# Performance work log

Measured on AMD Instinct MI355X. Metric: run time of the kernel, lower is better.

Reference implementation:

```python
import jax, jax.numpy as jnp
import numpy as np

H, D, K = 8, 512, 64
EPS = 1e-12


def _l2norm(x):
    # F.normalize(p=2, dim=-1): x / max(||x||_2, eps)
    n = jnp.sqrt(jnp.sum(x * x, axis=-1, keepdims=True))
    return x / jnp.maximum(n, EPS)


def setup_inputs() -> dict:
    key = jax.random.key(0)
    ks = jax.random.split(key, 8)
    S, B = 1024, 16
    scale = 1.0 / np.sqrt(D)
    return {
        "query": jax.random.normal(ks[0], (S, B, D), dtype=jnp.float32),
        "key": jax.random.normal(ks[1], (S, B, D), dtype=jnp.float32),
        "value": jax.random.normal(ks[2], (S, B, D), dtype=jnp.float32),
        # stacked per-head projection weights, torch Linear convention [out,in]
        "WQ": jax.random.uniform(ks[3], (H, K, D), jnp.float32, -scale, scale),
        "WK": jax.random.uniform(ks[4], (H, K, D), jnp.float32, -scale, scale),
        "WV": jax.random.uniform(ks[5], (H, K, D), jnp.float32, -scale, scale),
        "Wout": jax.random.uniform(ks[6], (D, H * K), jnp.float32,
                                   -1.0 / np.sqrt(H * K), 1.0 / np.sqrt(H * K)),
    }


def reference(query, key, value, WQ, WK, WV, Wout):
    temp = K ** 0.5
    # project all heads at once: [S,B,D] x [H,K,D] -> [B,H,S,K]
    wq = _l2norm(jnp.einsum("sbd,hkd->bhsk", query, WQ))
    wk = _l2norm(jnp.einsum("sbd,hkd->bhsk", key, WK))
    wv = _l2norm(jnp.einsum("sbd,hkd->bhsk", value, WV))
    # cosine-similarity attention scores [B,H,Sq,Sk]
    scores = jnp.einsum("bhsk,bhtk->bhst", wq, wk) / temp
    aff = jax.nn.softmax(scores, axis=-1)
    out = jnp.einsum("bhst,bhtk->bhsk", aff, wv)  # [B,H,S,K]
    # concat heads -> [S,B,H*K] (matches torch per-head concat on last dim)
    Sq, B = query.shape[0], query.shape[1]
    concat = out.transpose(2, 0, 1, 3).reshape(Sq, B, H * K)
    return concat @ Wout.T  # [S,B,D]
```

## Files before the change

kernel.cpp:

```cpp
#include <hip/hip_runtime.h>
#include <cstdint>
#include <cstddef>

typedef unsigned int u32;
typedef unsigned short u16;
typedef __attribute__((ext_vector_type(8))) short short8;
typedef __attribute__((ext_vector_type(4))) float f32x4;

#define S_LEN 1024
#define BATCH 16
#define NHEAD 8
#define DMODEL 512
#define KHD 64
#define NROW (S_LEN * BATCH)

__device__ __forceinline__ u16 f2bf(float f) {
    u32 u = __float_as_uint(f);
    return (u16)((u + 0x7fffu + ((u >> 16) & 1u)) >> 16);
}

__device__ __forceinline__ void gl_lds16(const void* g, void* l) {
    __builtin_amdgcn_global_load_lds(
        (const __attribute__((address_space(1))) void*)(uintptr_t)g,
        (__attribute__((address_space(3))) void*)(uintptr_t)l, 16, 0, 0);
}

__global__ __launch_bounds__(256) void wcvt_kernel(
    const float* __restrict__ WQ, const float* __restrict__ WK,
    const float* __restrict__ WV, const float* __restrict__ Wo,
    u16* __restrict__ dst)
{
    const int m = blockIdx.y;
    const float* __restrict__ src = (m == 0) ? WQ : (m == 1) ? WK : (m == 2) ? WV : Wo;
    const int idx = (blockIdx.x * 256 + threadIdx.x) * 4;
    const float4 v = *(const float4*)(src + idx);
    u16 r[4];
    r[0] = f2bf(v.x); r[1] = f2bf(v.y); r[2] = f2bf(v.z); r[3] = f2bf(v.w);
    *(uint2*)(dst + (size_t)m * DMODEL * DMODEL + idx) = *(uint2*)r;
}

template<int M>
__global__ __launch_bounds__(256) void gemm_kernel(
    const float* __restrict__ A0,
    const float* __restrict__ A1,
    const u16* __restrict__ Wb,
    u16* __restrict__ outN)
{
    __shared__ __align__(16) u16 Alds[128 * 64];
    __shared__ __align__(16) u16 Blds[128 * 64];

    const int tid  = threadIdx.x;
    const int wave = tid >> 6;
    const int lane = tid & 63;
    const int m16  = lane & 15;
    const int quad = lane >> 4;
    const int wm   = wave >> 1;
    const int wn   = wave & 1;
    const int n0   = blockIdx.y * 128;
    const int row0 = blockIdx.x * 128;
    const int z    = (M == 1) ? blockIdx.z : 0;
    const int bb   = (M == 2) ? blockIdx.z : 0;

    const float* __restrict__ A32 =
        (M == 1) ? (z ? A1 : A0) : (A0 + (size_t)bb * DMODEL);
    const size_t astr = (M == 2) ? (size_t)BATCH * DMODEL : (size_t)DMODEL;
    const u16* __restrict__ B = Wb + ((M == 1) ? (size_t)z * DMODEL * DMODEL : 0);

    f32x4 acc[4][4] = {};

    const int brow   = lane >> 3;
    const int bchunk = (lane & 7) ^ brow;
    const int acf    = lane & 7;

    for (int kt = 0; kt < DMODEL; kt += 64) {
        __syncthreads();
        {
            const u16* bp = B + (size_t)(n0 + wave * 32 + brow) * DMODEL + kt + bchunk * 8;
            u16* lb = &Blds[(wave * 32) * 64];
            float4 av[8];
#pragma unroll
            for (int j = 0; j < 8; j++) {
                const int rl = wave * 32 + (j & 3) * 8 + brow;
                const int cf = (j >> 2) * 8 + acf;
                av[j] = *(const float4*)(A32 + (size_t)(row0 + rl) * astr + kt + cf * 4);
            }
#pragma unroll
            for (int j = 0; j < 4; j++)
                gl_lds16(bp + (size_t)j * 8 * DMODEL, lb + j * 8 * 64);
#pragma unroll
            for (int j = 0; j < 8; j++) {
                const int rl = wave * 32 + (j & 3) * 8 + brow;
                const int cf = (j >> 2) * 8 + acf;
                u32 lo, hi;
                asm("v_cvt_pk_bf16_f32 %0, %1, %2" : "=v"(lo) : "v"(av[j].x), "v"(av[j].y));
                asm("v_cvt_pk_bf16_f32 %0, %1, %2" : "=v"(hi) : "v"(av[j].z), "v"(av[j].w));
                uint2 pk; pk.x = lo; pk.y = hi;
                *(uint2*)&Alds[rl * 64 + (((cf >> 1) ^ (rl & 7)) << 3) + ((cf & 1) << 2)] = pk;
            }
        }
        __syncthreads();

#pragma unroll
        for (int half = 0; half < 2; half++) {
            short8 af[4], bfr[4];
#pragma unroll
            for (int mt = 0; mt < 4; mt++)
                af[mt] = *(const short8*)&Alds[(wm * 64 + mt * 16 + m16) * 64 +
                                               (((half << 2) + quad) ^ (m16 & 7)) * 8];
#pragma unroll
            for (int nt = 0; nt < 4; nt++)
                bfr[nt] = *(const short8*)&Blds[(wn * 64 + nt * 16 + m16) * 64 +
                                                (((half << 2) + quad) ^ (m16 & 7)) * 8];
#pragma unroll
            for (int mt = 0; mt < 4; mt++)
#pragma unroll
                for (int nt = 0; nt < 4; nt++)
                    acc[mt][nt] = __builtin_amdgcn_mfma_f32_16x16x32_bf16(af[mt], bfr[nt], acc[mt][nt], 0, 0, 0);
        }
    }

    if (M == 1) {
        const int h = (n0 >> 6) + wn;
        u16* outZ = outN + (size_t)z * BATCH * NHEAD * S_LEN * KHD;
#pragma unroll
        for (int mt = 0; mt < 4; mt++) {
#pragma unroll
            for (int r = 0; r < 4; r++) {
                float ss = 0.0f;
#pragma unroll
                for (int nt = 0; nt < 4; nt++) ss += acc[mt][nt][r] * acc[mt][nt][r];
                ss += __shfl_xor(ss, 1);
                ss += __shfl_xor(ss, 2);
                ss += __shfl_xor(ss, 4);
                ss += __shfl_xor(ss, 8);
                const float sc = 1.0f / fmaxf(sqrtf(ss), 1e-12f);
                const int i = row0 + wm * 64 + mt * 16 + quad * 4 + r;
                const int s = i >> 4, b = i & 15;
                u16* op = outN + (size_t)z * BATCH * NHEAD * S_LEN * KHD +
                          (((size_t)b * NHEAD + h) * S_LEN + s) * KHD;
                (void)outZ;
#pragma unroll
                for (int nt = 0; nt < 4; nt++)
                    op[nt * 16 + m16] = f2bf(acc[mt][nt][r] * sc);
            }
        }
    } else {
        const int h = (n0 >> 6) + wn;
#pragma unroll
        for (int mt = 0; mt < 4; mt++) {
            float scl[4];
#pragma unroll
            for (int r = 0; r < 4; r++) {
                float ss = 0.0f;
#pragma unroll
                for (int nt = 0; nt < 4; nt++) ss += acc[mt][nt][r] * acc[mt][nt][r];
                ss += __shfl_xor(ss, 1);
                ss += __shfl_xor(ss, 2);
                ss += __shfl_xor(ss, 4);
                ss += __shfl_xor(ss, 8);
                scl[r] = 1.0f / fmaxf(sqrtf(ss), 1e-12f);
            }
            const int sbase = row0 + wm * 64 + mt * 16 + quad * 4;
#pragma unroll
            for (int nt = 0; nt < 4; nt++) {
                const int vcol = nt * 16 + m16;
                uint2 pk;
                pk.x = (u32)f2bf(acc[mt][nt][0] * scl[0]) |
                       ((u32)f2bf(acc[mt][nt][1] * scl[1]) << 16);
                pk.y = (u32)f2bf(acc[mt][nt][2] * scl[2]) |
                       ((u32)f2bf(acc[mt][nt][3] * scl[3]) << 16);
                u16* dp = outN + (((size_t)bb * NHEAD + h) * KHD + vcol) * S_LEN + sbase;
                *(uint2*)dp = pk;
            }
        }
    }
}

__global__ __launch_bounds__(512, 2) void gemm_out_kernel(
    const u16* __restrict__ Abf,
    const u16* __restrict__ Wb,
    float* __restrict__ outP)
{
    __shared__ __align__(16) u16 Alds[2][128 * 64];
    __shared__ __align__(16) u16 Blds[2][128 * 64];

    const int tid  = threadIdx.x;
    const int wave = tid >> 6;
    const int lane = tid & 63;
    const int m16  = lane & 15;
    const int quad = lane >> 4;
    const int wm   = wave >> 1;
    const int wn   = wave & 1;
    const int n0   = blockIdx.y * 128;
    const int row0 = blockIdx.x * 128;

    const int brow   = lane >> 3;
    const int bchunk = (lane & 7) ^ brow;

    f32x4 acc[2][4] = {};

    auto stage = [&](int kt, int b) {
        const int colc = kt + bchunk * 8;
        const int hh   = colc >> 6;
        const int kk   = colc & 63;
        u16* la = &Alds[b][(wave * 16) * 64];
#pragma unroll
        for (int j = 0; j < 2; j++) {
            const int i  = row0 + wave * 16 + j * 8 + brow;
            const int ss = i >> 4, bx = i & 15;
            gl_lds16(Abf + (((size_t)(bx * NHEAD + hh) * S_LEN + ss) * KHD + kk),
                     la + j * 8 * 64);
        }
        const u16* bp = Wb + (size_t)(n0 + wave * 16 + brow) * DMODEL + kt + bchunk * 8;
        u16* lb = &Blds[b][(wave * 16) * 64];
#pragma unroll
        for (int j = 0; j < 2; j++)
            gl_lds16(bp + (size_t)j * 8 * DMODEL, lb + j * 8 * 64);
    };
    auto compute = [&](int b) {
#pragma unroll
        for (int half = 0; half < 2; half++) {
            short8 af[2], bfr[4];
#pragma unroll
            for (int mt = 0; mt < 2; mt++)
                af[mt] = *(const short8*)&Alds[b][(wm * 32 + mt * 16 + m16) * 64 +
                                                  (((half << 2) + quad) ^ (m16 & 7)) * 8];
#pragma unroll
            for (int nt = 0; nt < 4; nt++)
                bfr[nt] = *(const short8*)&Blds[b][(wn * 64 + nt * 16 + m16) * 64 +
                                                   (((half << 2) + quad) ^ (m16 & 7)) * 8];
#pragma unroll
            for (int mt = 0; mt < 2; mt++)
#pragma unroll
                for (int nt = 0; nt < 4; nt++)
                    acc[mt][nt] = __builtin_amdgcn_mfma_f32_16x16x32_bf16(af[mt], bfr[nt], acc[mt][nt], 0, 0, 0);
        }
    };

    stage(0, 0);
    stage(64, 1);
    asm volatile("s_waitcnt vmcnt(4)" ::: "memory");
    __builtin_amdgcn_s_barrier();
    __builtin_amdgcn_sched_barrier(0);

#pragma unroll
    for (int t = 0; t < 8; t++) {
        compute(t & 1);
        if (t < 6) {
            __builtin_amdgcn_s_barrier();
            __builtin_amdgcn_sched_barrier(0);
            stage((t + 2) * 64, t & 1);
        }
        if (t < 7) {
            if (t < 6) asm volatile("s_waitcnt vmcnt(4)" ::: "memory");
            else       asm volatile("s_waitcnt vmcnt(0)" ::: "memory");
            __builtin_amdgcn_s_barrier();
            __builtin_amdgcn_sched_barrier(0);
        }
    }

#pragma unroll
    for (int mt = 0; mt < 2; mt++) {
#pragma unroll
        for (int r = 0; r < 4; r++) {
            const int i = row0 + wm * 32 + mt * 16 + quad * 4 + r;
            float* op = outP + (size_t)i * DMODEL + n0 + wn * 64;
#pragma unroll
            for (int nt = 0; nt < 4; nt++)
                op[nt * 16 + m16] = acc[mt][nt][r];
        }
    }
}

__global__ __launch_bounds__(256, 2) void attn_kernel(
    const u16* __restrict__ wq, const u16* __restrict__ wk, const u16* __restrict__ wvT,
    u16* __restrict__ Xout)
{
    __shared__ __align__(16) u16 Klds[2][64 * 64];
    __shared__ __align__(16) u16 Vlds[2][64 * 64];
    __shared__ __align__(16) u16 Plds[4][4][16 * 32];

    const int tid  = threadIdx.x;
    const int wave = tid >> 6;
    const int lane = tid & 63;
    const int m16  = lane & 15;
    const int quad = lane >> 4;
    const int bh   = blockIdx.x;
    const int qt   = blockIdx.y;

    const u16* Qb = wq  + (size_t)bh * S_LEN * KHD;
    const u16* Kb = wk  + (size_t)bh * S_LEN * KHD;
    const u16* Vb = wvT + (size_t)bh * KHD * S_LEN;

    const int qr0 = qt * 256 + wave * 64;
    short8 qf[4][2];
#pragma unroll
    for (int qb = 0; qb < 4; qb++) {
        qf[qb][0] = *(const short8*)(Qb + (size_t)(qr0 + qb * 16 + m16) * KHD + quad * 8);
        qf[qb][1] = *(const short8*)(Qb + (size_t)(qr0 + qb * 16 + m16) * KHD + 32 + quad * 8);
    }

    short8 ones;
#pragma unroll
    for (int j = 0; j < 8; j++) ones[j] = (short)0x3F80;

    f32x4 o[4][4] = {};
    f32x4 ls[4]   = {};
    const float C1 = 0.125f, C2 = 0.0078125f;

    const int srow   = lane >> 3;
    const int schunk = (lane & 7) ^ srow;
    const int r0     = wave * 8 + srow;
    const int pswz   = (m16 >> 1) & 3;

    gl_lds16(Kb + (size_t)r0 * KHD + schunk * 8,               &Klds[0][(wave * 8) * 64]);
    gl_lds16(Kb + (size_t)(r0 + 32) * KHD + schunk * 8,        &Klds[0][(wave * 8 + 32) * 64]);
    gl_lds16(Vb + (size_t)r0 * S_LEN + schunk * 8,             &Vlds[0][(wave * 8) * 64]);
    gl_lds16(Vb + (size_t)(r0 + 32) * S_LEN + schunk * 8,      &Vlds[0][(wave * 8 + 32) * 64]);
    __syncthreads();

    for (int it = 0; it < S_LEN / 64; it++) {
        const int cur = it & 1;

        if (it + 1 < S_LEN / 64) {
            const int nxt = cur ^ 1;
            const int kt0 = (it + 1) * 64;
            gl_lds16(Kb + (size_t)(kt0 + r0) * KHD + schunk * 8,        &Klds[nxt][(wave * 8) * 64]);
            gl_lds16(Kb + (size_t)(kt0 + r0 + 32) * KHD + schunk * 8,   &Klds[nxt][(wave * 8 + 32) * 64]);
            gl_lds16(Vb + (size_t)r0 * S_LEN + kt0 + schunk * 8,        &Vlds[nxt][(wave * 8) * 64]);
            gl_lds16(Vb + (size_t)(r0 + 32) * S_LEN + kt0 + schunk * 8, &Vlds[nxt][(wave * 8 + 32) * 64]);
        }

#pragma unroll
        for (int cc = 0; cc < 2; cc++) {
#pragma unroll
            for (int mm = 0; mm < 2; mm++) {
                const int mt = cc * 2 + mm;
                const short8 kf0 = *(const short8*)&Klds[cur][(mt * 16 + m16) * 64 + (quad ^ (m16 & 7)) * 8];
                const short8 kf1 = *(const short8*)&Klds[cur][(mt * 16 + m16) * 64 + ((4 + quad) ^ (m16 & 7)) * 8];
#pragma unroll
                for (int qb = 0; qb < 4; qb++) {
                    f32x4 s = {};
                    s = __builtin_amdgcn_mfma_f32_16x16x32_bf16(kf0, qf[qb][0], s, 0, 0, 0);
                    s = __builtin_amdgcn_mfma_f32_16x16x32_bf16(kf1, qf[qb][1], s, 0, 0, 0);
                    u32 up[4];
#pragma unroll
                    for (int r = 0; r < 4; r++) {
                        const float y = s[r];
                        const float p = fmaf(fmaf(C2, y, C1), y, 1.0f);
                        up[r] = __float_as_uint(p);
                    }
                    uint2 pk;
                    pk.x = __builtin_amdgcn_perm(up[1], up[0], 0x07060302u);
                    pk.y = __builtin_amdgcn_perm(up[3], up[2], 0x07060302u);
                    *(uint2*)((char*)&Plds[wave][qb][0] + m16 * 64 +
                              ((((mm << 1) + (quad >> 1)) ^ pswz) << 4) + ((quad & 1) << 3)) = pk;
                }
            }

            short8 vfr[4];
#pragma unroll
            for (int vt = 0; vt < 4; vt++)
                vfr[vt] = *(const short8*)&Vlds[cur][(vt * 16 + m16) * 64 +
                                                     (((cc << 2) + quad) ^ (m16 & 7)) * 8];
            __builtin_amdgcn_s_setprio(1);
#pragma unroll
            for (int qb = 0; qb < 4; qb++) {
                const short8 pb = *(const short8*)((const char*)&Plds[wave][qb][0] + m16 * 64 +
                                                   ((quad ^ pswz) << 4));
                ls[qb] = __builtin_amdgcn_mfma_f32_16x16x32_bf16(ones, pb, ls[qb], 0, 0, 0);
#pragma unroll
                for (int vt = 0; vt < 4; vt++)
                    o[qb][vt] = __builtin_amdgcn_mfma_f32_16x16x32_bf16(vfr[vt], pb, o[qb][vt], 0, 0, 0);
            }
            __builtin_amdgcn_s_setprio(0);
        }

        __syncthreads();
    }

    u16* outB = Xout + (size_t)bh * S_LEN * KHD;
#pragma unroll
    for (int qb = 0; qb < 4; qb++) {
        const float inv = 1.0f / ls[qb][0];
        const int qrow = qr0 + qb * 16 + m16;
        u16* cp = outB + (size_t)qrow * KHD;
#pragma unroll
        for (int vt = 0; vt < 4; vt++) {
            uint2 pk;
            pk.x = (u32)f2bf(o[qb][vt][0] * inv) | ((u32)f2bf(o[qb][vt][1] * inv) << 16);
            pk.y = (u32)f2bf(o[qb][vt][2] * inv) | ((u32)f2bf(o[qb][vt][3] * inv) << 16);
            *(uint2*)(cp + vt * 16 + quad * 4) = pk;
        }
    }
}

extern "C" void kernel_launch(void* const* d_in, const int* in_sizes, int n_in,
                              void* d_out, int out_size, void* d_ws, size_t ws_size,
                              hipStream_t stream) {
    const float* q    = (const float*)d_in[0];
    const float* k    = (const float*)d_in[1];
    const float* v    = (const float*)d_in[2];
    const float* WQ   = (const float*)d_in[3];
    const float* WK   = (const float*)d_in[4];
    const float* WV   = (const float*)d_in[5];
    const float* Wout = (const float*)d_in[6];
    float* out = (float*)d_out;

    const size_t per = (size_t)BATCH * NHEAD * S_LEN * KHD;
    u16* wsQKV = (u16*)d_ws;
    u16* wsW   = wsQKV + 3 * per;

    wcvt_kernel<<<dim3(256, 4), 256, 0, stream>>>(WQ, WK, WV, Wout, wsW);

    gemm_kernel<1><<<dim3(NROW / 128, DMODEL / 128, 2), 256, 0, stream>>>(
        q, k, wsW, wsQKV);

    gemm_kernel<2><<<dim3(S_LEN / 128, DMODEL / 128, BATCH), 256, 0, stream>>>(
        v, nullptr, wsW + (size_t)2 * DMODEL * DMODEL, wsQKV + 2 * per);

    attn_kernel<<<dim3(BATCH * NHEAD, S_LEN / 256), 256, 0, stream>>>(
        wsQKV, wsQKV + per, wsQKV + 2 * per, wsQKV);

    gemm_out_kernel<<<dim3(NROW / 128, DMODEL / 128), 512, 0, stream>>>(
        wsQKV, wsW + (size_t)3 * DMODEL * DMODEL, out);
}
```

Baseline: 238.9 us.

## Merge Q/K/V projections into one double-buffered direct-to-LDS GEMM kernel

The two templated projection GEMM launches become a single 1536-block kernel that picks Q, K or V work from the block index. The fp32 activations now go straight from global memory into LDS through global_load_lds, with a two-stage buffer over 32-wide k-tiles, and are converted to bf16 after the LDS read instead of in registers before the LDS write. Blocks use 512 threads, each wave computing a 32x64 tile, which should raise occupancy and overlap the loads with the MFMAs. The cost is twice the LDS bytes per element for fp32 A, conversion repeated by each wave that reads a row, and manual vmcnt and barrier bookkeeping that must stay correct.

Result: slower. 243.7 us (+2.0%).

```diff
diff --git a/kernel.cpp b/kernel.cpp
--- a/kernel.cpp
+++ b/kernel.cpp
@@ -39,15 +39,13 @@
     *(uint2*)(dst + (size_t)m * DMODEL * DMODEL + idx) = *(uint2*)r;
 }
 
-template<int M>
-__global__ __launch_bounds__(256) void gemm_kernel(
-    const float* __restrict__ A0,
-    const float* __restrict__ A1,
-    const u16* __restrict__ Wb,
+__global__ __launch_bounds__(512, 6) void proj_kernel(
+    const float* __restrict__ q, const float* __restrict__ k,
+    const float* __restrict__ v, const u16* __restrict__ Wb,
     u16* __restrict__ outN)
 {
-    __shared__ __align__(16) u16 Alds[128 * 64];
-    __shared__ __align__(16) u16 Blds[128 * 64];
+    __shared__ __align__(16) float Alds[2][128 * 32];
+    __shared__ __align__(16) u16   Blds[2][128 * 32];
 
     const int tid  = threadIdx.x;
     const int wave = tid >> 6;
@@ -56,74 +54,94 @@
     const int quad = lane >> 4;
     const int wm   = wave >> 1;
     const int wn   = wave & 1;
-    const int n0   = blockIdx.y * 128;
-    const int row0 = blockIdx.x * 128;
-    const int z    = (M == 1) ? blockIdx.z : 0;
-    const int bb   = (M == 2) ? blockIdx.z : 0;
-
-    const float* __restrict__ A32 =
-        (M == 1) ? (z ? A1 : A0) : (A0 + (size_t)bb * DMODEL);
-    const size_t astr = (M == 2) ? (size_t)BATCH * DMODEL : (size_t)DMODEL;
-    const u16* __restrict__ B = Wb + ((M == 1) ? (size_t)z * DMODEL * DMODEL : 0);
-
-    f32x4 acc[4][4] = {};
-
-    const int brow   = lane >> 3;
-    const int bchunk = (lane & 7) ^ brow;
-    const int acf    = lane & 7;
-
-    for (int kt = 0; kt < DMODEL; kt += 64) {
-        __syncthreads();
+
+    const int bid  = blockIdx.x;
+    const bool isM1 = bid < 1024;
+    int z, bx, by, bb;
+    if (isM1) { z = bid >> 9; by = (bid >> 7) & 3; bx = bid & 127; bb = 0; }
+    else { const int r = bid - 1024; z = 2; bb = r >> 5; by = (r >> 3) & 3; bx = r & 7; }
+
+    const int row0 = bx * 128;
+    const int n0   = by * 128;
+    const float* __restrict__ A32 = isM1 ? (z ? k : q) : (v + (size_t)bb * DMODEL);
+    const size_t astr = isM1 ? (size_t)DMODEL : (size_t)BATCH * DMODEL;
+    const u16* __restrict__ B = Wb + (size_t)z * DMODEL * DMODEL;
+
+    f32x4 acc[2][4] = {};
+
+    const int ar  = lane >> 3, ac = lane & 7;
+    const int alc = ac ^ ar;
+    const int br  = lane >> 2, bc = lane & 3;
+    const int blc = bc ^ (br & 3);
+
+    auto stage = [&](int kt, int bufi) {
+#pragma unroll
+        for (int j = 0; j < 2; j++) {
+            const int row = wave * 16 + j * 8 + ar;
+            gl_lds16(A32 + (size_t)(row0 + row) * astr + kt + alc * 4,
+                     &Alds[bufi][(wave * 16 + j * 8) * 32]);
+        }
         {
-            const u16* bp = B + (size_t)(n0 + wave * 32 + brow) * DMODEL + kt + bchunk * 8;
-            u16* lb = &Blds[(wave * 32) * 64];
-            float4 av[8];
-#pragma unroll
-            for (int j = 0; j < 8; j++) {
-                const int rl = wave * 32 + (j & 3) * 8 + brow;
-                const int cf = (j >> 2) * 8 + acf;
-                av[j] = *(const float4*)(A32 + (size_t)(row0 + rl) * astr + kt + cf * 4);
-            }
-#pragma unroll
-            for (int j = 0; j < 4; j++)
-                gl_lds16(bp + (size_t)j * 8 * DMODEL, lb + j * 8 * 64);
-#pragma unroll
-            for (int j = 0; j < 8; j++) {
-                const int rl = wave * 32 + (j & 3) * 8 + brow;
-                const int cf = (j >> 2) * 8 + acf;
-                u32 lo, hi;
-                asm("v_cvt_pk_bf16_f32 %0, %1, %2" : "=v"(lo) : "v"(av[j].x), "v"(av[j].y));
-                asm("v_cvt_pk_bf16_f32 %0, %1, %2" : "=v"(hi) : "v"(av[j].z), "v"(av[j].w));
-                uint2 pk; pk.x = lo; pk.y = hi;
-                *(uint2*)&Alds[rl * 64 + (((cf >> 1) ^ (rl & 7)) << 3) + ((cf & 1) << 2)] = pk;
-            }
-        }
-        __syncthreads();
-
-#pragma unroll
-        for (int half = 0; half < 2; half++) {
-            short8 af[4], bfr[4];
-#pragma unroll
-            for (int mt = 0; mt < 4; mt++)
-                af[mt] = *(const short8*)&Alds[(wm * 64 + mt * 16 + m16) * 64 +
-                                               (((half << 2) + quad) ^ (m16 & 7)) * 8];
+            const int row = wave * 16 + br;
+            gl_lds16(B + (size_t)(n0 + row) * DMODEL + kt + blc * 8,
+                     &Blds[bufi][(wave * 16) * 32]);
+        }
+    };
+    auto compute = [&](int bufi) {
+        short8 af[2], bfr[4];
+#pragma unroll
+        for (int mt = 0; mt < 2; mt++) {
+            const int row = wm * 32 + mt * 16 + m16;
+            const int pc  = (quad << 1) ^ (m16 & 7);
+            const float4 lo = *(const float4*)&Alds[bufi][row * 32 + pc * 4];
+            const float4 hi = *(const float4*)&Alds[bufi][row * 32 + (pc ^ 1) * 4];
+            u32 pkv[4];
+            asm("v_cvt_pk_bf16_f32 %0, %1, %2" : "=v"(pkv[0]) : "v"(lo.x), "v"(lo.y));
+            asm("v_cvt_pk_bf16_f32 %0, %1, %2" : "=v"(pkv[1]) : "v"(lo.z), "v"(lo.w));
+            asm("v_cvt_pk_bf16_f32 %0, %1, %2" : "=v"(pkv[2]) : "v"(hi.x), "v"(hi.y));
+            asm("v_cvt_pk_bf16_f32 %0, %1, %2" : "=v"(pkv[3]) : "v"(hi.z), "v"(hi.w));
+            af[mt] = *(const short8*)pkv;
+        }
+#pragma unroll
+        for (int nt = 0; nt < 4; nt++) {
+            const int row = wn * 64 + nt * 16 + m16;
+            const int pc  = quad ^ (m16 & 3);
+            bfr[nt] = *(const short8*)&Blds[bufi][row * 32 + pc * 8];
+        }
+#pragma unroll
+        for (int mt = 0; mt < 2; mt++)
 #pragma unroll
             for (int nt = 0; nt < 4; nt++)
-                bfr[nt] = *(const short8*)&Blds[(wn * 64 + nt * 16 + m16) * 64 +
-                                                (((half << 2) + quad) ^ (m16 & 7)) * 8];
-#pragma unroll
-            for (int mt = 0; mt < 4; mt++)
-#pragma unroll
-                for (int nt = 0; nt < 4; nt++)
-                    acc[mt][nt] = __builtin_amdgcn_mfma_f32_16x16x32_bf16(af[mt], bfr[nt], acc[mt][nt], 0, 0, 0);
-        }
-    }
-
-    if (M == 1) {
-        const int h = (n0 >> 6) + wn;
-        u16* outZ = outN + (size_t)z * BATCH * NHEAD * S_LEN * KHD;
-#pragma unroll
-        for (int mt = 0; mt < 4; mt++) {
+                acc[mt][nt] = __builtin_amdgcn_mfma_f32_16x16x32_bf16(af[mt], bfr[nt], acc[mt][nt], 0, 0, 0);
+    };
+
+    stage(0, 0);
+    stage(32, 1);
+    asm volatile("s_waitcnt vmcnt(3)" ::: "memory");
+    __builtin_amdgcn_s_barrier();
+    __builtin_amdgcn_sched_barrier(0);
+
+#pragma unroll
+    for (int t = 0; t < 16; t++) {
+        compute(t & 1);
+        if (t < 14) {
+            __builtin_amdgcn_s_barrier();
+            __builtin_amdgcn_sched_barrier(0);
+            stage((t + 2) * 32, t & 1);
+        }
+        if (t < 15) {
+            if (t < 14) asm volatile("s_waitcnt vmcnt(3)" ::: "memory");
+            else        asm volatile("s_waitcnt vmcnt(0)" ::: "memory");
+            __builtin_amdgcn_s_barrier();
+            __builtin_amdgcn_sched_barrier(0);
+        }
+    }
+
+    const int h = (n0 >> 6) + wn;
+    u16* outZ = outN + (size_t)z * ((size_t)BATCH * NHEAD * S_LEN * KHD);
+    if (isM1) {
+#pragma unroll
+        for (int mt = 0; mt < 2; mt++) {
 #pragma unroll
             for (int r = 0; r < 4; r++) {
                 float ss = 0.0f;
@@ -134,20 +152,17 @@
                 ss += __shfl_xor(ss, 4);
                 ss += __shfl_xor(ss, 8);
                 const float sc = 1.0f / fmaxf(sqrtf(ss), 1e-12f);
-                const int i = row0 + wm * 64 + mt * 16 + quad * 4 + r;
-                const int s = i >> 4, b = i & 15;
-                u16* op = outN + (size_t)z * BATCH * NHEAD * S_LEN * KHD +
-                          (((size_t)b * NHEAD + h) * S_LEN + s) * KHD;
-                (void)outZ;
+                const int i = row0 + wm * 32 + mt * 16 + quad * 4 + r;
+                const int s = i >> 4, bq = i & 15;
+                u16* op = outZ + (((size_t)bq * NHEAD + h) * S_LEN + s) * KHD;
 #pragma unroll
                 for (int nt = 0; nt < 4; nt++)
                     op[nt * 16 + m16] = f2bf(acc[mt][nt][r] * sc);
             }
         }
     } else {
-        const int h = (n0 >> 6) + wn;
-#pragma unroll
-        for (int mt = 0; mt < 4; mt++) {
+#pragma unroll
+        for (int mt = 0; mt < 2; mt++) {
             float scl[4];
 #pragma unroll
             for (int r = 0; r < 4; r++) {
@@ -160,7 +175,7 @@
                 ss += __shfl_xor(ss, 8);
                 scl[r] = 1.0f / fmaxf(sqrtf(ss), 1e-12f);
             }
-            const int sbase = row0 + wm * 64 + mt * 16 + quad * 4;
+            const int sbase = row0 + wm * 32 + mt * 16 + quad * 4;
 #pragma unroll
             for (int nt = 0; nt < 4; nt++) {
                 const int vcol = nt * 16 + m16;
@@ -169,7 +184,7 @@
                        ((u32)f2bf(acc[mt][nt][1] * scl[1]) << 16);
                 pk.y = (u32)f2bf(acc[mt][nt][2] * scl[2]) |
                        ((u32)f2bf(acc[mt][nt][3] * scl[3]) << 16);
-                u16* dp = outN + (((size_t)bb * NHEAD + h) * KHD + vcol) * S_LEN + sbase;
+                u16* dp = outZ + (((size_t)bb * NHEAD + h) * KHD + vcol) * S_LEN + sbase;
                 *(uint2*)dp = pk;
             }
         }
@@ -413,11 +428,7 @@
 
     wcvt_kernel<<<dim3(256, 4), 256, 0, stream>>>(WQ, WK, WV, Wout, wsW);
 
-    gemm_kernel<1><<<dim3(NROW / 128, DMODEL / 128, 2), 256, 0, stream>>>(
-        q, k, wsW, wsQKV);
-
-    gemm_kernel<2><<<dim3(S_LEN / 128, DMODEL / 128, BATCH), 256, 0, stream>>>(
-        v, nullptr, wsW + (size_t)2 * DMODEL * DMODEL, wsQKV + 2 * per);
+    proj_kernel<<<dim3(1536), 512, 0, stream>>>(q, k, v, wsW, wsQKV);
 
     attn_kernel<<<dim3(BATCH * NHEAD, S_LEN / 256), 256, 0, stream>>>(
         wsQKV, wsQKV + per, wsQKV + 2 * per, wsQKV);
```
